# Performance work log

Measured on AMD Instinct MI355X. Metric: run time of the kernel, lower is better.

Reference implementation:

```python
import jax, jax.numpy as jnp
import numpy as np

B, T, D = 8, 4096, 1024
H, HD = 8, 128            # head_dim = ceil(D/H)
P = H * HD                # proj_dim = 1024
OUT = 1024
WIN, STRIDE = 64, 32


def _window_index(seq_len, win, stride):
    # mirrors the Python start-list construction in RollingAttentionPooling.forward
    starts = list(range(0, max(1, seq_len), stride))
    if starts and starts[-1] + win < seq_len:
        starts.append(seq_len - win)
    starts = sorted(set(max(0, s) for s in starts))
    idx = np.asarray(starts)[:, None] + np.arange(win)[None, :]
    valid = idx < seq_len
    idx = np.minimum(idx, seq_len - 1)
    return jnp.asarray(idx, dtype=jnp.int32), jnp.asarray(valid)


def setup_inputs() -> dict:
    key = jax.random.key(0)
    k0, k1, k2, k3 = jax.random.split(key, 4)
    x = jax.random.normal(k0, (B, T, D), dtype=jnp.float32)
    w_kv = jax.random.normal(k1, (D, 2 * P), dtype=jnp.float32) * 0.02
    query = jax.random.normal(k2, (H, HD), dtype=jnp.float32)
    w_out_w = jax.random.normal(k3, (OUT, P), dtype=jnp.float32) * 0.02
    w_out_b = jnp.zeros((OUT,), dtype=jnp.float32)
    return {"x": x, "w_kv": w_kv, "query": query, "w_out_w": w_out_w, "w_out_b": w_out_b}


def reference(x, w_kv, query, w_out_w, w_out_b):
    bsz, seq_len, _ = x.shape
    # K/V projection computed once for the whole sequence (same math as
    # recomputing per-window, since windows are slices of x).
    kv = (x @ w_kv).reshape(bsz, seq_len, 2, H, HD)
    k = kv[:, :, 0]                                   # (B, T, H, HD)
    v = kv[:, :, 1]                                   # (B, T, H, HD)
    logits = jnp.einsum('bthd,hd->bht', k, query) / jnp.sqrt(jnp.float32(HD))

    idx, valid = _window_index(seq_len, WIN, STRIDE)
    lw = logits[:, :, idx]
    lw = jnp.where(valid[None, None], lw, -jnp.inf)
    scores = jax.nn.softmax(lw.astype(jnp.float32), axis=-1).astype(v.dtype)
    vw = v[:, idx]
    pooled = jnp.einsum('bhwt,bwthd->bwhd', scores, vw)
    pooled = pooled.reshape(bsz, idx.shape[0], P)     # (B, W, P)
    out_w = pooled @ w_out_w.T + w_out_b              # (B, W, OUT)
    return out_w.mean(axis=1)                         # (B, OUT)
```

## Files before the change

kernel.cpp:

```cpp
#include <hip/hip_runtime.h>

#define B_ 8
#define T_ 4096
#define D_ 1024
#define H_ 8
#define HD_ 128
#define P_ 1024
#define OUT_ 1024
#define W_ 128
#define NC_ 64
#define CH_ 64
#define NPC_ 64
#define PCH_ 16

#define TRL_ 128
#define DKL_ 128
#define NKC_ (D_ / DKL_)
#define LSTR_ (DKL_ + 4)

__global__ void __launch_bounds__(256) k_qproj(const float* __restrict__ w_kv,
                                               const float* __restrict__ query,
                                               float* __restrict__ qp) {
  int d = blockIdx.x;
  int t = threadIdx.x;
  float4 wv = ((const float4*)(w_kv + (size_t)d * (2 * P_)))[t];
  float4 qv = ((const float4*)query)[t];
  float a = wv.x * qv.x + wv.y * qv.y + wv.z * qv.z + wv.w * qv.w;
#pragma unroll
  for (int off = 16; off; off >>= 1) a += __shfl_xor(a, off, 64);
  if ((t & 31) == 0) {
    int h = t >> 5;
    qp[h * D_ + d] = a * 0.08838834764831845f;
  }
}

__global__ void __launch_bounds__(256) k_logits(const float* __restrict__ x,
                                                const float* __restrict__ qp,
                                                float* __restrict__ logits) {
  __shared__ float s_x[TRL_ * LSTR_];
  __shared__ float s_q[H_ * LSTR_];
  __shared__ float s_out[H_][TRL_];
  const int t = threadIdx.x;
  const int r = t >> 3;
  const int h = t & 7;
  const int R0 = blockIdx.x * TRL_;
  const int b = R0 >> 12, t0 = R0 & (T_ - 1);

  const float4* xg = (const float4*)x;
  const float4* qg = (const float4*)qp;

  float4 stx[16];
  float4 stq;
#pragma unroll
  for (int q = 0; q < 16; ++q) {
    int i = t + 256 * q;
    int row = i >> 5, c4 = i & 31;
    stx[q] = xg[((size_t)(R0 + row) << 8) + c4];
  }
  {
    int hh = t >> 5, c4 = t & 31;
    stq = qg[(hh << 8) + c4];
  }

  float4 a0 = make_float4(0.f, 0.f, 0.f, 0.f);
  float4 a1 = make_float4(0.f, 0.f, 0.f, 0.f);
  float4 a2 = make_float4(0.f, 0.f, 0.f, 0.f);
  float4 a3 = make_float4(0.f, 0.f, 0.f, 0.f);
  for (int kc = 0; kc < NKC_; ++kc) {
    __syncthreads();
#pragma unroll
    for (int q = 0; q < 16; ++q) {
      int i = t + 256 * q;
      int row = i >> 5, c4 = i & 31;
      *(float4*)&s_x[row * LSTR_ + 4 * c4] = stx[q];
    }
    {
      int hh = t >> 5, c4 = t & 31;
      *(float4*)&s_q[hh * LSTR_ + 4 * c4] = stq;
    }
    __syncthreads();
    if (kc + 1 < NKC_) {
      int kb = (kc + 1) << 5;
#pragma unroll
      for (int q = 0; q < 16; ++q) {
        int i = t + 256 * q;
        int row = i >> 5, c4 = i & 31;
        stx[q] = xg[((size_t)(R0 + row) << 8) + kb + c4];
      }
      int hh = t >> 5, c4 = t & 31;
      stq = qg[(hh << 8) + kb + c4];
    }
#pragma unroll
    for (int k4 = 0; k4 < DKL_ / 4; ++k4) {
      float4 qv = *(const float4*)&s_q[h * LSTR_ + 4 * k4];
      float4 x0 = *(const float4*)&s_x[(r)      * LSTR_ + 4 * k4];
      float4 x1 = *(const float4*)&s_x[(r + 32) * LSTR_ + 4 * k4];
      float4 x2 = *(const float4*)&s_x[(r + 64) * LSTR_ + 4 * k4];
      float4 x3 = *(const float4*)&s_x[(r + 96) * LSTR_ + 4 * k4];
      a0.x += x0.x * qv.x; a0.y += x0.y * qv.y; a0.z += x0.z * qv.z; a0.w += x0.w * qv.w;
      a1.x += x1.x * qv.x; a1.y += x1.y * qv.y; a1.z += x1.z * qv.z; a1.w += x1.w * qv.w;
      a2.x += x2.x * qv.x; a2.y += x2.y * qv.y; a2.z += x2.z * qv.z; a2.w += x2.w * qv.w;
      a3.x += x3.x * qv.x; a3.y += x3.y * qv.y; a3.z += x3.z * qv.z; a3.w += x3.w * qv.w;
    }
  }
  s_out[h][r]      = (a0.x + a0.y) + (a0.z + a0.w);
  s_out[h][r + 32] = (a1.x + a1.y) + (a1.z + a1.w);
  s_out[h][r + 64] = (a2.x + a2.y) + (a2.z + a2.w);
  s_out[h][r + 96] = (a3.x + a3.y) + (a3.z + a3.w);
  __syncthreads();
  {
    int hh = t >> 5, j = t & 31;
    float4 val = *(const float4*)&s_out[hh][4 * j];
    *(float4*)&logits[(((size_t)(b * H_ + hh)) << 12) + t0 + 4 * j] = val;
  }
}

__global__ void __launch_bounds__(256) k_yacc(const float* __restrict__ x,
                                              const float* __restrict__ logits,
                                              float* __restrict__ partial) {
  int c = blockIdx.x;
  int b = blockIdx.y;
  int t0 = c * CH_;
  int W0 = (t0 >> 5) - 1;
  __shared__ float sw[CH_][H_];
  __shared__ float sm[4][H_], srs[4][H_];
  int tid = threadIdx.x;
  if (tid < 3 * H_) {
    int wi = tid >> 3, h = tid & 7;
    int w = W0 + wi;
    if (w >= 0 && w < W_) {
      const float* L = logits + (((size_t)(b * H_ + h)) << 12) + (w << 5);
      int cnt = min(64, T_ - (w << 5));
      float m = -1e30f;
#pragma unroll 8
      for (int i = 0; i < cnt; ++i) m = fmaxf(m, L[i]);
      float s = 0.f;
#pragma unroll 8
      for (int i = 0; i < cnt; ++i) s += __expf(L[i] - m);
      sm[wi][h] = m;
      srs[wi][h] = 1.0f / s;
    }
  }
  __syncthreads();
  const float invW = 1.0f / (float)W_;
  for (int i = tid; i < H_ * CH_; i += 256) {
    int h = i >> 6, tt = i & 63;
    int tg = t0 + tt;
    float l = logits[(((size_t)(b * H_ + h)) << 12) + tg];
    int w1 = tg >> 5;
    int rel = w1 - W0;
    float acc = __expf(l - sm[rel][h]) * srs[rel][h];
    if (w1 > 0) acc += __expf(l - sm[rel - 1][h]) * srs[rel - 1][h];
    sw[tt][h] = acc * invW;
  }
  __syncthreads();
  float4 acc[H_];
#pragma unroll
  for (int h = 0; h < H_; ++h) acc[h] = make_float4(0.f, 0.f, 0.f, 0.f);
  const float4* xb = (const float4*)(x + ((size_t)b * T_ + t0) * D_);
  for (int tt0 = 0; tt0 < CH_; tt0 += 8) {
    float4 xv[8];
#pragma unroll
    for (int j = 0; j < 8; ++j) xv[j] = xb[(tt0 + j) * (D_ / 4) + tid];
#pragma unroll
    for (int j = 0; j < 8; ++j) {
      float4 wa = *(const float4*)&sw[tt0 + j][0];
      float4 wb = *(const float4*)&sw[tt0 + j][4];
      acc[0].x += wa.x * xv[j].x; acc[0].y += wa.x * xv[j].y; acc[0].z += wa.x * xv[j].z; acc[0].w += wa.x * xv[j].w;
      acc[1].x += wa.y * xv[j].x; acc[1].y += wa.y * xv[j].y; acc[1].z += wa.y * xv[j].z; acc[1].w += wa.y * xv[j].w;
      acc[2].x += wa.z * xv[j].x; acc[2].y += wa.z * xv[j].y; acc[2].z += wa.z * xv[j].z; acc[2].w += wa.z * xv[j].w;
      acc[3].x += wa.w * xv[j].x; acc[3].y += wa.w * xv[j].y; acc[3].z += wa.w * xv[j].z; acc[3].w += wa.w * xv[j].w;
      acc[4].x += wb.x * xv[j].x; acc[4].y += wb.x * xv[j].y; acc[4].z += wb.x * xv[j].z; acc[4].w += wb.x * xv[j].w;
      acc[5].x += wb.y * xv[j].x; acc[5].y += wb.y * xv[j].y; acc[5].z += wb.y * xv[j].z; acc[5].w += wb.y * xv[j].w;
      acc[6].x += wb.z * xv[j].x; acc[6].y += wb.z * xv[j].y; acc[6].z += wb.z * xv[j].z; acc[6].w += wb.z * xv[j].w;
      acc[7].x += wb.w * xv[j].x; acc[7].y += wb.w * xv[j].y; acc[7].z += wb.w * xv[j].z; acc[7].w += wb.w * xv[j].w;
    }
  }
  float4* pp = (float4*)(partial + (((size_t)(c * B_ + b) * H_) << 10));
#pragma unroll
  for (int h = 0; h < H_; ++h) pp[h * (D_ / 4) + tid] = acc[h];
}

__global__ void __launch_bounds__(256) k_reduce_y(const float* __restrict__ partial,
                                                  float* __restrict__ y) {
  int i = blockIdx.x * blockDim.x + threadIdx.x;
  float4 a = make_float4(0.f, 0.f, 0.f, 0.f);
  const float4* p = (const float4*)partial;
#pragma unroll 8
  for (int c = 0; c < NC_; ++c) {
    float4 v = p[(size_t)c * (B_ * H_ * D_ / 4) + i];
    a.x += v.x; a.y += v.y; a.z += v.z; a.w += v.w;
  }
  ((float4*)y)[i] = a;
}

__global__ void __launch_bounds__(256) k_pooled_part(const float* __restrict__ y,
                                                     const float* __restrict__ w_kv,
                                                     float* __restrict__ ppart) {
  int c = blockIdx.x;
  int d0 = c * PCH_;
  int t = threadIdx.x;
  int h = t >> 5;
  __shared__ float sy[PCH_][B_ * H_];
  for (int i = t; i < PCH_ * B_ * H_; i += 256) {
    int dd = i >> 6, bh = i & 63;
    sy[dd][bh] = y[((size_t)bh << 10) + d0 + dd];
  }
  __syncthreads();
  float4 acc[B_];
#pragma unroll
  for (int b = 0; b < B_; ++b) acc[b] = make_float4(0.f, 0.f, 0.f, 0.f);
#pragma unroll
  for (int dd = 0; dd < PCH_; ++dd) {
    float4 wv = ((const float4*)(w_kv + (size_t)(d0 + dd) * (2 * P_) + P_))[t];
#pragma unroll
    for (int b = 0; b < B_; ++b) {
      float yv = sy[dd][b * H_ + h];
      acc[b].x += yv * wv.x; acc[b].y += yv * wv.y;
      acc[b].z += yv * wv.z; acc[b].w += yv * wv.w;
    }
  }
#pragma unroll
  for (int b = 0; b < B_; ++b)
    ((float4*)(ppart + (((size_t)c * B_ + b) << 10)))[t] = acc[b];
}

__global__ void __launch_bounds__(256) k_reduce_pooled(const float* __restrict__ ppart,
                                                       float* __restrict__ pooled) {
  int i = blockIdx.x * 256 + threadIdx.x;
  int b = i >> 8, p4 = i & 255;
  float4 a = make_float4(0.f, 0.f, 0.f, 0.f);
  const float4* p = (const float4*)ppart;
#pragma unroll 8
  for (int c = 0; c < NPC_; ++c) {
    float4 v = p[((c * B_ + b) << 8) + p4];
    a.x += v.x; a.y += v.y; a.z += v.z; a.w += v.w;
  }
  ((float4*)pooled)[i] = a;
}

__global__ void __launch_bounds__(256) k_out(const float* __restrict__ pooled,
                                             const float* __restrict__ w_out_w,
                                             const float* __restrict__ w_out_b,
                                             float* __restrict__ out) {
  int wid = threadIdx.x >> 6, lane = threadIdx.x & 63;
  int o = blockIdx.x * 4 + wid;
  const float4* wr = (const float4*)(w_out_w + (size_t)o * P_);
  float4 wv[4];
#pragma unroll
  for (int j = 0; j < 4; ++j) wv[j] = wr[lane + 64 * j];
  float res[B_];
#pragma unroll
  for (int b = 0; b < B_; ++b) {
    const float4* pb = (const float4*)(pooled + b * P_);
    float a = 0.f;
#pragma unroll
    for (int j = 0; j < 4; ++j) {
      float4 pv = pb[lane + 64 * j];
      a += wv[j].x * pv.x + wv[j].y * pv.y + wv[j].z * pv.z + wv[j].w * pv.w;
    }
#pragma unroll
    for (int off = 32; off; off >>= 1) a += __shfl_down(a, off, 64);
    res[b] = a;
  }
  if (lane == 0) {
    float bias = w_out_b[o];
#pragma unroll
    for (int b = 0; b < B_; ++b) out[b * OUT_ + o] = res[b] + bias;
  }
}

extern "C" void kernel_launch(void* const* d_in, const int* in_sizes, int n_in,
                              void* d_out, int out_size, void* d_ws, size_t ws_size,
                              hipStream_t stream) {
  const float* x       = (const float*)d_in[0];
  const float* w_kv    = (const float*)d_in[1];
  const float* query   = (const float*)d_in[2];
  const float* w_out_w = (const float*)d_in[3];
  const float* w_out_b = (const float*)d_in[4];
  float* out = (float*)d_out;

  float* ws = (float*)d_ws;
  float* qp      = ws;
  float* logits  = qp + H_ * D_;
  float* partial = logits + B_ * H_ * T_;
  float* y       = partial + (size_t)NC_ * B_ * H_ * D_;
  float* pooled  = y + B_ * H_ * D_;
  float* ppart   = partial;

  k_qproj<<<D_, 256, 0, stream>>>(w_kv, query, qp);
  k_logits<<<B_ * T_ / TRL_, 256, 0, stream>>>(x, qp, logits);
  k_yacc<<<dim3(NC_, B_), 256, 0, stream>>>(x, logits, partial);
  k_reduce_y<<<(B_ * H_ * D_ / 4) / 256, 256, 0, stream>>>(partial, y);
  k_pooled_part<<<NPC_, 256, 0, stream>>>(y, w_kv, ppart);
  k_reduce_pooled<<<(B_ * P_ / 4) / 256, 256, 0, stream>>>(ppart, pooled);
  k_out<<<OUT_ / 4, 256, 0, stream>>>(pooled, w_out_w, w_out_b, out);
}
```

Before: 283.5 us.

## Restructure logits kernel to stream x rows from global with LDS-resident query

The logits kernel no longer stages 128-row x tiles through shared memory with double buffering. Each block now loads the full projected query (8x1024) into LDS, handles 32 rows, and has 16 lanes per row stream x directly from global memory with a one-step register prefetch. It then combines the 8 head partial sums with a butterfly shuffle reduction. This drops the per-chunk LDS writes and barriers on x and launches four times as many blocks, at the cost of reloading the 32KB query into LDS in every block and scalar logits stores.

New measurement: 261.0 us. 1.09x faster.

```diff
diff --git a/kernel.cpp b/kernel.cpp
--- a/kernel.cpp
+++ b/kernel.cpp
@@ -13,10 +13,7 @@
 #define NPC_ 64
 #define PCH_ 16
 
-#define TRL_ 128
-#define DKL_ 128
-#define NKC_ (D_ / DKL_)
-#define LSTR_ (DKL_ + 4)
+#define TRL_ 32
 
 __global__ void __launch_bounds__(256) k_qproj(const float* __restrict__ w_kv,
                                                const float* __restrict__ query,
@@ -37,81 +34,60 @@
 __global__ void __launch_bounds__(256) k_logits(const float* __restrict__ x,
                                                 const float* __restrict__ qp,
                                                 float* __restrict__ logits) {
-  __shared__ float s_x[TRL_ * LSTR_];
-  __shared__ float s_q[H_ * LSTR_];
-  __shared__ float s_out[H_][TRL_];
+  __shared__ float s_q[H_ * D_];
+  __shared__ float s_out[H_][TRL_ + 1];
   const int t = threadIdx.x;
-  const int r = t >> 3;
-  const int h = t & 7;
+  for (int i = t; i < H_ * D_ / 4; i += 256)
+    ((float4*)s_q)[i] = ((const float4*)qp)[i];
+  __syncthreads();
+
+  const int w = t >> 6;
+  const int l = t & 63;
+  const int rr = l >> 4;
+  const int c16 = l & 15;
   const int R0 = blockIdx.x * TRL_;
-  const int b = R0 >> 12, t0 = R0 & (T_ - 1);
-
-  const float4* xg = (const float4*)x;
-  const float4* qg = (const float4*)qp;
-
-  float4 stx[16];
-  float4 stq;
-#pragma unroll
-  for (int q = 0; q < 16; ++q) {
-    int i = t + 256 * q;
-    int row = i >> 5, c4 = i & 31;
-    stx[q] = xg[((size_t)(R0 + row) << 8) + c4];
-  }
-  {
-    int hh = t >> 5, c4 = t & 31;
-    stq = qg[(hh << 8) + c4];
-  }
-
-  float4 a0 = make_float4(0.f, 0.f, 0.f, 0.f);
-  float4 a1 = make_float4(0.f, 0.f, 0.f, 0.f);
-  float4 a2 = make_float4(0.f, 0.f, 0.f, 0.f);
-  float4 a3 = make_float4(0.f, 0.f, 0.f, 0.f);
-  for (int kc = 0; kc < NKC_; ++kc) {
-    __syncthreads();
-#pragma unroll
-    for (int q = 0; q < 16; ++q) {
-      int i = t + 256 * q;
-      int row = i >> 5, c4 = i & 31;
-      *(float4*)&s_x[row * LSTR_ + 4 * c4] = stx[q];
-    }
-    {
-      int hh = t >> 5, c4 = t & 31;
-      *(float4*)&s_q[hh * LSTR_ + 4 * c4] = stq;
-    }
-    __syncthreads();
-    if (kc + 1 < NKC_) {
-      int kb = (kc + 1) << 5;
-#pragma unroll
-      for (int q = 0; q < 16; ++q) {
-        int i = t + 256 * q;
-        int row = i >> 5, c4 = i & 31;
-        stx[q] = xg[((size_t)(R0 + row) << 8) + kb + c4];
+  const bool b0 = (c16 & 1), b1 = (c16 & 2), b2 = (c16 & 4);
+  const int hsel = (c16 & 1) * 4 + ((c16 >> 1) & 1) * 2 + ((c16 >> 2) & 1);
+
+#pragma unroll
+  for (int it = 0; it < 2; ++it) {
+    const int lrow = w * 8 + it * 4 + rr;
+    const int row = R0 + lrow;
+    const float4* xr = (const float4*)(x + ((size_t)row << 10));
+    float4 p4[H_];
+#pragma unroll
+    for (int h = 0; h < H_; ++h) p4[h] = make_float4(0.f, 0.f, 0.f, 0.f);
+    float4 xv = xr[c16];
+#pragma unroll
+    for (int kc = 0; kc < 16; ++kc) {
+      float4 xc = xv;
+      if (kc < 15) xv = xr[(kc + 1) * 16 + c16];
+      const float* qb = s_q + kc * 64 + c16 * 4;
+#pragma unroll
+      for (int h = 0; h < H_; ++h) {
+        float4 qv = *(const float4*)(qb + h * D_);
+        p4[h].x += xc.x * qv.x; p4[h].y += xc.y * qv.y;
+        p4[h].z += xc.z * qv.z; p4[h].w += xc.w * qv.w;
       }
-      int hh = t >> 5, c4 = t & 31;
-      stq = qg[(hh << 8) + kb + c4];
-    }
-#pragma unroll
-    for (int k4 = 0; k4 < DKL_ / 4; ++k4) {
-      float4 qv = *(const float4*)&s_q[h * LSTR_ + 4 * k4];
-      float4 x0 = *(const float4*)&s_x[(r)      * LSTR_ + 4 * k4];
-      float4 x1 = *(const float4*)&s_x[(r + 32) * LSTR_ + 4 * k4];
-      float4 x2 = *(const float4*)&s_x[(r + 64) * LSTR_ + 4 * k4];
-      float4 x3 = *(const float4*)&s_x[(r + 96) * LSTR_ + 4 * k4];
-      a0.x += x0.x * qv.x; a0.y += x0.y * qv.y; a0.z += x0.z * qv.z; a0.w += x0.w * qv.w;
-      a1.x += x1.x * qv.x; a1.y += x1.y * qv.y; a1.z += x1.z * qv.z; a1.w += x1.w * qv.w;
-      a2.x += x2.x * qv.x; a2.y += x2.y * qv.y; a2.z += x2.z * qv.z; a2.w += x2.w * qv.w;
-      a3.x += x3.x * qv.x; a3.y += x3.y * qv.y; a3.z += x3.z * qv.z; a3.w += x3.w * qv.w;
-    }
-  }
-  s_out[h][r]      = (a0.x + a0.y) + (a0.z + a0.w);
-  s_out[h][r + 32] = (a1.x + a1.y) + (a1.z + a1.w);
-  s_out[h][r + 64] = (a2.x + a2.y) + (a2.z + a2.w);
-  s_out[h][r + 96] = (a3.x + a3.y) + (a3.z + a3.w);
+    }
+    float p[H_];
+#pragma unroll
+    for (int h = 0; h < H_; ++h) p[h] = (p4[h].x + p4[h].y) + (p4[h].z + p4[h].w);
+    float v0 = (b0 ? p[4] : p[0]) + __shfl_xor(b0 ? p[0] : p[4], 1, 64);
+    float v1 = (b0 ? p[5] : p[1]) + __shfl_xor(b0 ? p[1] : p[5], 1, 64);
+    float v2 = (b0 ? p[6] : p[2]) + __shfl_xor(b0 ? p[2] : p[6], 1, 64);
+    float v3 = (b0 ? p[7] : p[3]) + __shfl_xor(b0 ? p[3] : p[7], 1, 64);
+    float w0 = (b1 ? v2 : v0) + __shfl_xor(b1 ? v0 : v2, 2, 64);
+    float w1 = (b1 ? v3 : v1) + __shfl_xor(b1 ? v1 : v3, 2, 64);
+    float u = (b2 ? w1 : w0) + __shfl_xor(b2 ? w0 : w1, 4, 64);
+    u += __shfl_xor(u, 8, 64);
+    if (c16 < 8) s_out[hsel][lrow] = u;
+  }
   __syncthreads();
   {
     int hh = t >> 5, j = t & 31;
-    float4 val = *(const float4*)&s_out[hh][4 * j];
-    *(float4*)&logits[(((size_t)(b * H_ + hh)) << 12) + t0 + 4 * j] = val;
+    int b = R0 >> 12, t0 = R0 & (T_ - 1);
+    logits[(((size_t)(b * H_ + hh)) << 12) + t0 + j] = s_out[hh][j];
   }
 }
 
```
